# Performance work log

Measured on AMD Instinct MI355X. Metric: run time of the kernel, lower is better.

## Reference

```python
import jax, jax.numpy as jnp
import numpy as np

B, E = 256, 512
C, K = 8192, 10          # n_class, n_center
LMD = 10.0
INV_GAMMA = 10.0         # 1 / gamma, gamma = 0.1
TAU = 0.2
MARGIN = 0.01


def setup_inputs() -> dict:
    key = jax.random.key(0)
    k1, k2, k3 = jax.random.split(key, 3)
    embeddings = jax.random.normal(k1, (B, E), dtype=jnp.float32)
    labels = jax.random.randint(k2, (B,), 0, C, dtype=jnp.int64)
    fc = jax.random.normal(k3, (C * K, E), dtype=jnp.float32)
    return {"embeddings": embeddings, "labels": labels, "fc": fc}


def reference(embeddings, labels, fc):
    # L2-normalize centers (rows of fc), like F.normalize(fc, p=2, dim=1)
    norm = jnp.sqrt(jnp.sum(fc * fc, axis=1, keepdims=True))
    w = fc / jnp.maximum(norm, 1e-12)

    # similarity to every center: [B, C, K]
    x = (embeddings @ w.T).reshape(B, C, K)
    prob = jax.nn.softmax(INV_GAMMA * x, axis=2)
    h = jnp.sum(prob * x, axis=2)  # [B, C] soft-pooled class similarity

    # subtract margin on ground-truth class, then cross-entropy
    rows = jnp.arange(B)
    margin_m = jnp.zeros_like(h).at[rows, labels].set(MARGIN)
    logits = LMD * (h - margin_m)
    logp = jax.nn.log_softmax(logits, axis=1)
    loss_cls = -jnp.mean(logp[rows, labels])

    # regularizer: batched per-class center gram, replaces python loop over C
    wc = w.reshape(C, K, E)
    sub = 1.0 - jnp.einsum('cke,cje->ckj', wc, wc)   # [C, K, K]
    sub = jnp.where(sub <= 0.0, 1e-10, sub)
    mask = jnp.triu(jnp.ones((K, K), dtype=bool), k=1)  # strict upper triangle
    safe = jnp.where(mask, 2.0 * sub, 1.0)
    reg = jnp.sum(jnp.where(mask, jnp.sqrt(safe), 0.0))
    reg = reg / (C * K * (K - 1.0))
    return loss_cls + TAU * reg
```

## Files before the change

### kernel.cpp

```cpp
#include <hip/hip_runtime.h>


typedef __bf16 bf16;
typedef bf16 bf16x8 __attribute__((ext_vector_type(8)));
typedef float f32x4 __attribute__((ext_vector_type(4)));

#define NCLASS 8192
#define KC 10
#define EDIM 512
#define BATCH 256

__device__ inline void load_lds16(const void* g, void* l) {
    __builtin_amdgcn_global_load_lds(
        (const __attribute__((address_space(1))) void*)g,
        (__attribute__((address_space(3))) void*)l, 16, 0, 0);
}

__global__ __launch_bounds__(256) void prep_kernel(
    const float* __restrict__ fc, bf16* __restrict__ w,
    float* __restrict__ gram_part)
{
    __shared__ float rows[KC * EDIM];
    __shared__ float s_invn[KC];
    __shared__ float s_wsum[4];
    const int c = blockIdx.x;
    const int t = threadIdx.x;
    const int wave = t >> 6, lane = t & 63;

    const float4* src = (const float4*)(fc + (size_t)c * (KC * EDIM));
    float4* rows4 = (float4*)rows;
    #pragma unroll
    for (int i = 0; i < 5; ++i) rows4[t + i * 256] = src[t + i * 256];
    __syncthreads();

    for (int r = wave; r < KC; r += 4) {
        float s = 0.f;
        #pragma unroll
        for (int j = 0; j < 8; ++j) {
            float v = rows[r * EDIM + lane + j * 64];
            s += v * v;
        }
        #pragma unroll
        for (int off = 32; off; off >>= 1) s += __shfl_xor(s, off);
        if (lane == 0) s_invn[r] = 1.0f / fmaxf(sqrtf(s), 1e-12f);
    }
    __syncthreads();

    bf16x8* dst = (bf16x8*)(w + (size_t)c * (KC * EDIM));
    #pragma unroll
    for (int p = 0; p < 3; ++p) {
        int j = t + p * 256;
        if (j < 640) {
            int r = j >> 6;
            float inv = s_invn[r];
            float4 a = *(const float4*)(rows + j * 8);
            float4 b = *(const float4*)(rows + j * 8 + 4);
            bf16x8 v;
            v[0] = (bf16)(a.x * inv); v[1] = (bf16)(a.y * inv);
            v[2] = (bf16)(a.z * inv); v[3] = (bf16)(a.w * inv);
            v[4] = (bf16)(b.x * inv); v[5] = (bf16)(b.y * inv);
            v[6] = (bf16)(b.z * inv); v[7] = (bf16)(b.w * inv);
            dst[j] = v;
        }
    }

    float part = 0.f;
    for (int p = wave; p < 45; p += 4) {
        int i = 0, pp = p;
        while (pp >= 9 - i) { pp -= 9 - i; ++i; }
        int j = i + 1 + pp;
        float s = 0.f;
        #pragma unroll
        for (int u = 0; u < 8; ++u)
            s += rows[i * EDIM + lane + u * 64] * rows[j * EDIM + lane + u * 64];
        #pragma unroll
        for (int off = 32; off; off >>= 1) s += __shfl_xor(s, off);
        if (lane == 0) {
            float sub = 1.0f - s * s_invn[i] * s_invn[j];
            if (sub <= 0.0f) sub = 1e-10f;
            part += sqrtf(2.0f * sub);
        }
    }
    if (lane == 0) s_wsum[wave] = part;
    __syncthreads();
    if (t == 0) gram_part[c] = s_wsum[0] + s_wsum[1] + s_wsum[2] + s_wsum[3];
}

__global__ __launch_bounds__(256) void conv_kernel(
    const float* __restrict__ e, bf16* __restrict__ out, float4* __restrict__ zpad)
{
    int i = blockIdx.x * 256 + threadIdx.x;
    if (blockIdx.x == 0 && threadIdx.x < 8) {
        float4 z = {0.f, 0.f, 0.f, 0.f};
        zpad[threadIdx.x] = z;
    }
    float4 a = ((const float4*)e)[i * 2];
    float4 b = ((const float4*)e)[i * 2 + 1];
    bf16x8 v;
    v[0] = (bf16)a.x; v[1] = (bf16)a.y; v[2] = (bf16)a.z; v[3] = (bf16)a.w;
    v[4] = (bf16)b.x; v[5] = (bf16)b.y; v[6] = (bf16)b.z; v[7] = (bf16)b.w;
    ((bf16x8*)out)[i] = v;
}

__global__ __launch_bounds__(512) void gemm_h_kernel(
    const bf16* __restrict__ W,
    const bf16* __restrict__ A,
    const bf16* __restrict__ zpad,
    float* __restrict__ h)
{
    __shared__ bf16 Ws[128 * 32];
    __shared__ bf16 Es[256 * 32];
    const int tid = threadIdx.x;
    const int wave = tid >> 6, lane = tid & 63;
    const int wm = wave & 1, wn = wave >> 1;

    f32x4 acc[4][4];
    #pragma unroll
    for (int mt = 0; mt < 4; ++mt)
        #pragma unroll
        for (int nt = 0; nt < 4; ++nt)
            acc[mt][nt] = (f32x4){0.f, 0.f, 0.f, 0.f};

    const int lrow = lane >> 2;
    const int lcol = (lane & 3) * 8;

    const int cls = blockIdx.x * 8 + wave;
    const bool real = (lrow < KC);
    const bf16* wsrc0 = real
        ? W + ((size_t)cls * KC + lrow) * EDIM + lcol
        : zpad + lcol;
    const int wstep = real ? 1 : 0;

    for (int kb = 0; kb < EDIM; kb += 32) {
        load_lds16(wsrc0 + (size_t)kb * wstep, Ws + (wave * 16) * 32);
        #pragma unroll
        for (int p = 0; p < 2; ++p) {
            int row = p * 128 + wave * 16 + lrow;
            load_lds16(A + row * EDIM + kb + lcol,
                       Es + (p * 128 + wave * 16) * 32);
        }
        __syncthreads();

        const int q8 = (lane >> 4) * 8;
        bf16x8 wf[4], ef[4];
        #pragma unroll
        for (int mt = 0; mt < 4; ++mt)
            wf[mt] = *(const bf16x8*)&Ws[(wm * 64 + mt * 16 + (lane & 15)) * 32 + q8];
        #pragma unroll
        for (int nt = 0; nt < 4; ++nt)
            ef[nt] = *(const bf16x8*)&Es[(wn * 64 + nt * 16 + (lane & 15)) * 32 + q8];
        #pragma unroll
        for (int mt = 0; mt < 4; ++mt)
            #pragma unroll
            for (int nt = 0; nt < 4; ++nt)
                acc[mt][nt] = __builtin_amdgcn_mfma_f32_16x16x32_bf16(
                    wf[mt], ef[nt], acc[mt][nt], 0, 0, 0);
        __syncthreads();
    }

    const int col = lane & 15;
    const int quad = lane >> 4;
    #pragma unroll
    for (int mt = 0; mt < 4; ++mt) {
        int oc = blockIdx.x * 8 + wm * 4 + mt;
        #pragma unroll
        for (int nt = 0; nt < 4; ++nt) {
            int b = wn * 64 + nt * 16 + col;
            float xm = -1e30f;
            #pragma unroll
            for (int r = 0; r < 4; ++r)
                if (quad * 4 + r < KC) xm = fmaxf(xm, acc[mt][nt][r]);
            xm = fmaxf(xm, __shfl_xor(xm, 16));
            xm = fmaxf(xm, __shfl_xor(xm, 32));
            float s1 = 0.f, s2 = 0.f;
            #pragma unroll
            for (int r = 0; r < 4; ++r) {
                if (quad * 4 + r < KC) {
                    float x = acc[mt][nt][r];
                    float e = __expf(10.0f * (x - xm));
                    s1 += e; s2 += e * x;
                }
            }
            s1 += __shfl_xor(s1, 16); s1 += __shfl_xor(s1, 32);
            s2 += __shfl_xor(s2, 16); s2 += __shfl_xor(s2, 32);
            if (quad == 0) h[(size_t)b * NCLASS + oc] = s2 / s1;
        }
    }
}

__global__ __launch_bounds__(256) void ce_kernel(
    const float* __restrict__ h, const int* __restrict__ labels,
    float* __restrict__ ce_part)
{
    __shared__ float redm[4];
    __shared__ float reds[4];
    const int b = blockIdx.x, t = threadIdx.x;
    const int wave = t >> 6, lane = t & 63;
    const int lbl = labels[b];
    const float* hb = h + (size_t)b * NCLASS;

    float lg_cache[32];
    float mx = -1e30f;
    #pragma unroll
    for (int k = 0; k < 32; ++k) {
        int c = t + k * 256;
        float lg = 10.0f * hb[c];
        if (c == lbl) lg -= 0.1f;
        lg_cache[k] = lg;
        mx = fmaxf(mx, lg);
    }
    #pragma unroll
    for (int off = 32; off; off >>= 1) mx = fmaxf(mx, __shfl_xor(mx, off));
    if (lane == 0) redm[wave] = mx;
    __syncthreads();
    mx = fmaxf(fmaxf(redm[0], redm[1]), fmaxf(redm[2], redm[3]));

    float s = 0.f;
    #pragma unroll
    for (int k = 0; k < 32; ++k) s += __expf(lg_cache[k] - mx);
    #pragma unroll
    for (int off = 32; off; off >>= 1) s += __shfl_xor(s, off);
    if (lane == 0) reds[wave] = s;
    __syncthreads();
    if (t == 0) {
        s = reds[0] + reds[1] + reds[2] + reds[3];
        float logit_l = 10.0f * (hb[lbl] - 0.01f);
        ce_part[b] = mx + logf(s) - logit_l;
    }
}

__global__ __launch_bounds__(256) void final_kernel(
    const float* __restrict__ gram_part, const float* __restrict__ ce_part,
    float* __restrict__ out)
{
    __shared__ float red[4];
    const int t = threadIdx.x, wave = t >> 6, lane = t & 63;
    float g = 0.f;
    #pragma unroll
    for (int i = 0; i < 32; ++i) g += gram_part[t + i * 256];
    float val = ce_part[t] * (1.0f / 256.0f)
              + g * (0.2f / 737280.0f);
    #pragma unroll
    for (int off = 32; off; off >>= 1) val += __shfl_xor(val, off);
    if (lane == 0) red[wave] = val;
    __syncthreads();
    if (t == 0) out[0] = red[0] + red[1] + red[2] + red[3];
}

extern "C" void kernel_launch(void* const* d_in, const int* in_sizes, int n_in,
                              void* d_out, int out_size, void* d_ws, size_t ws_size,
                              hipStream_t stream) {
    const float* emb    = (const float*)d_in[0];
    const int*   labels = (const int*)d_in[1];
    const float* fc     = (const float*)d_in[2];
    float* out = (float*)d_out;

    char* ws = (char*)d_ws;
    bf16*  w         = (bf16*)ws;
    bf16*  embb      = (bf16*)(ws + 83886080);
    bf16*  zpad      = (bf16*)(ws + 84148224);
    float* h         = (float*)(ws + 84148352);
    float* gram_part = (float*)(ws + 92536960);
    float* ce_part   = (float*)(ws + 92569728);

    prep_kernel<<<NCLASS, 256, 0, stream>>>(fc, w, gram_part);
    conv_kernel<<<64, 256, 0, stream>>>(emb, embb, (float4*)zpad);
    gemm_h_kernel<<<131072 / 128, 512, 0, stream>>>(w, embb, zpad, h);
    ce_kernel<<<BATCH, 256, 0, stream>>>(h, labels, ce_part);
    final_kernel<<<1, 256, 0, stream>>>(gram_part, ce_part, out);
}
```

Measured before the change: 310.2 us.

## Pack class centers densely into GEMM tile, removing zero-padded rows

```diff
diff --git a/kernel.cpp b/kernel.cpp
--- a/kernel.cpp
+++ b/kernel.cpp
@@ -87,13 +87,9 @@
 }
 
 __global__ __launch_bounds__(256) void conv_kernel(
-    const float* __restrict__ e, bf16* __restrict__ out, float4* __restrict__ zpad)
+    const float* __restrict__ e, bf16* __restrict__ out)
 {
     int i = blockIdx.x * 256 + threadIdx.x;
-    if (blockIdx.x == 0 && threadIdx.x < 8) {
-        float4 z = {0.f, 0.f, 0.f, 0.f};
-        zpad[threadIdx.x] = z;
-    }
     float4 a = ((const float4*)e)[i * 2];
     float4 b = ((const float4*)e)[i * 2 + 1];
     bf16x8 v;
@@ -105,54 +101,49 @@
 __global__ __launch_bounds__(512) void gemm_h_kernel(
     const bf16* __restrict__ W,
     const bf16* __restrict__ A,
-    const bf16* __restrict__ zpad,
     float* __restrict__ h)
 {
-    __shared__ bf16 Ws[128 * 32];
+    __shared__ bf16 Ws[80 * 32];
     __shared__ bf16 Es[256 * 32];
     const int tid = threadIdx.x;
     const int wave = tid >> 6, lane = tid & 63;
-    const int wm = wave & 1, wn = wave >> 1;
-
-    f32x4 acc[4][4];
-    #pragma unroll
-    for (int mt = 0; mt < 4; ++mt)
-        #pragma unroll
-        for (int nt = 0; nt < 4; ++nt)
+
+    f32x4 acc[5][2];
+    #pragma unroll
+    for (int mt = 0; mt < 5; ++mt)
+        #pragma unroll
+        for (int nt = 0; nt < 2; ++nt)
             acc[mt][nt] = (f32x4){0.f, 0.f, 0.f, 0.f};
 
-    const int lrow = lane >> 2;
-    const int lcol = (lane & 3) * 8;
-
-    const int cls = blockIdx.x * 8 + wave;
-    const bool real = (lrow < KC);
-    const bf16* wsrc0 = real
-        ? W + ((size_t)cls * KC + lrow) * EDIM + lcol
-        : zpad + lcol;
-    const int wstep = real ? 1 : 0;
+    const size_t g0 = (size_t)blockIdx.x * 80;
+    const int srow = lane >> 2;
+    const int scol = (lane & 3) * 8;
 
     for (int kb = 0; kb < EDIM; kb += 32) {
-        load_lds16(wsrc0 + (size_t)kb * wstep, Ws + (wave * 16) * 32);
+        if (wave < 5)
+            load_lds16(W + (g0 + (wave << 4) + srow) * EDIM + kb + scol,
+                       Ws + ((wave << 4) * 32));
         #pragma unroll
         for (int p = 0; p < 2; ++p) {
-            int row = p * 128 + wave * 16 + lrow;
-            load_lds16(A + row * EDIM + kb + lcol,
+            int row = p * 128 + wave * 16 + srow;
+            load_lds16(A + row * EDIM + kb + scol,
                        Es + (p * 128 + wave * 16) * 32);
         }
         __syncthreads();
 
         const int q8 = (lane >> 4) * 8;
-        bf16x8 wf[4], ef[4];
-        #pragma unroll
-        for (int mt = 0; mt < 4; ++mt)
-            wf[mt] = *(const bf16x8*)&Ws[(wm * 64 + mt * 16 + (lane & 15)) * 32 + q8];
-        #pragma unroll
-        for (int nt = 0; nt < 4; ++nt)
-            ef[nt] = *(const bf16x8*)&Es[(wn * 64 + nt * 16 + (lane & 15)) * 32 + q8];
-        #pragma unroll
-        for (int mt = 0; mt < 4; ++mt)
+        const int fr = lane & 15;
+        bf16x8 wf[5], ef[2];
+        #pragma unroll
+        for (int mt = 0; mt < 5; ++mt)
+            wf[mt] = *(const bf16x8*)&Ws[(mt * 16 + fr) * 32 + q8];
+        #pragma unroll
+        for (int nt = 0; nt < 2; ++nt)
+            ef[nt] = *(const bf16x8*)&Es[(wave * 32 + nt * 16 + fr) * 32 + q8];
+        #pragma unroll
+        for (int mt = 0; mt < 5; ++mt)
             #pragma unroll
-            for (int nt = 0; nt < 4; ++nt)
+            for (int nt = 0; nt < 2; ++nt)
                 acc[mt][nt] = __builtin_amdgcn_mfma_f32_16x16x32_bf16(
                     wf[mt], ef[nt], acc[mt][nt], 0, 0, 0);
         __syncthreads();
@@ -160,30 +151,52 @@
 
     const int col = lane & 15;
     const int quad = lane >> 4;
-    #pragma unroll
-    for (int mt = 0; mt < 4; ++mt) {
-        int oc = blockIdx.x * 8 + wm * 4 + mt;
-        #pragma unroll
-        for (int nt = 0; nt < 4; ++nt) {
-            int b = wn * 64 + nt * 16 + col;
+    const int cb = blockIdx.x * 8;
+    #pragma unroll
+    for (int nt = 0; nt < 2; ++nt) {
+        int b = wave * 32 + nt * 16 + col;
+        float hval[8];
+        #pragma unroll
+        for (int c = 0; c < 8; ++c) {
             float xm = -1e30f;
             #pragma unroll
-            for (int r = 0; r < 4; ++r)
-                if (quad * 4 + r < KC) xm = fmaxf(xm, acc[mt][nt][r]);
+            for (int mt = 0; mt < 5; ++mt) {
+                if (10 * c + 10 > 16 * mt && 10 * c < 16 * mt + 16) {
+                    #pragma unroll
+                    for (int rg = 0; rg < 4; ++rg) {
+                        int r = 16 * mt + 4 * quad + rg;
+                        if (r >= 10 * c && r < 10 * c + 10)
+                            xm = fmaxf(xm, acc[mt][nt][rg]);
+                    }
+                }
+            }
             xm = fmaxf(xm, __shfl_xor(xm, 16));
             xm = fmaxf(xm, __shfl_xor(xm, 32));
             float s1 = 0.f, s2 = 0.f;
             #pragma unroll
-            for (int r = 0; r < 4; ++r) {
-                if (quad * 4 + r < KC) {
-                    float x = acc[mt][nt][r];
-                    float e = __expf(10.0f * (x - xm));
-                    s1 += e; s2 += e * x;
+            for (int mt = 0; mt < 5; ++mt) {
+                if (10 * c + 10 > 16 * mt && 10 * c < 16 * mt + 16) {
+                    #pragma unroll
+                    for (int rg = 0; rg < 4; ++rg) {
+                        int r = 16 * mt + 4 * quad + rg;
+                        if (r >= 10 * c && r < 10 * c + 10) {
+                            float x = acc[mt][nt][rg];
+                            float e = __expf(10.0f * (x - xm));
+                            s1 += e; s2 += e * x;
+                        }
+                    }
                 }
             }
             s1 += __shfl_xor(s1, 16); s1 += __shfl_xor(s1, 32);
             s2 += __shfl_xor(s2, 16); s2 += __shfl_xor(s2, 32);
-            if (quad == 0) h[(size_t)b * NCLASS + oc] = s2 / s1;
+            hval[c] = s2 / s1;
+        }
+        if (quad == 0) {
+            float4 v0 = {hval[0], hval[1], hval[2], hval[3]};
+            float4 v1 = {hval[4], hval[5], hval[6], hval[7]};
+            float4* dst = (float4*)&h[(size_t)b * NCLASS + cb];
+            dst[0] = v0;
+            dst[1] = v1;
         }
     }
 }
@@ -258,14 +271,13 @@
     char* ws = (char*)d_ws;
     bf16*  w         = (bf16*)ws;
     bf16*  embb      = (bf16*)(ws + 83886080);
-    bf16*  zpad      = (bf16*)(ws + 84148224);
     float* h         = (float*)(ws + 84148352);
     float* gram_part = (float*)(ws + 92536960);
     float* ce_part   = (float*)(ws + 92569728);
 
     prep_kernel<<<NCLASS, 256, 0, stream>>>(fc, w, gram_part);
-    conv_kernel<<<64, 256, 0, stream>>>(emb, embb, (float4*)zpad);
-    gemm_h_kernel<<<131072 / 128, 512, 0, stream>>>(w, embb, zpad, h);
+    conv_kernel<<<64, 256, 0, stream>>>(emb, embb);
+    gemm_h_kernel<<<81920 / 80, 512, 0, stream>>>(w, embb, h);
     ce_kernel<<<BATCH, 256, 0, stream>>>(h, labels, ce_part);
     final_kernel<<<1, 256, 0, stream>>>(gram_part, ce_part, out);
 }
```

After: 306.2 us. No clear change (-1.3%).
